# Kernel tuning notes

Measured on AMD Instinct MI355X. Metric: run time of the kernel, lower is better.

Reference implementation:

```python
import jax, jax.numpy as jnp
import numpy as np

EPS = 1e-5
LEAK = 0.1
NPOINT = 4096
NSAMPLE = 32


def setup_inputs() -> dict:
    key = jax.random.key(0)
    ks = jax.random.split(key, 6)
    B, N, Cin = 2, 16384, 64
    ch = [Cin + 3, 64, 64, 128]
    xyz = jax.random.normal(ks[0], (B, 3, N), jnp.float32)
    points = jax.random.normal(ks[1], (B, Cin, N), jnp.float32)
    W0 = jax.random.normal(ks[2], (ch[1], ch[0]), jnp.float32) * 0.05
    W1 = jax.random.normal(ks[3], (ch[2], ch[1]), jnp.float32) * 0.05
    W2 = jax.random.normal(ks[4], (ch[3], ch[2]), jnp.float32) * 0.05
    return dict(
        xyz=xyz, points=points, W0=W0, W1=W1, W2=W2,
        g0=jnp.ones((ch[1],), jnp.float32), b0=jnp.zeros((ch[1],), jnp.float32),
        g1=jnp.ones((ch[2],), jnp.float32), b1=jnp.zeros((ch[2],), jnp.float32),
        g2=jnp.ones((ch[3],), jnp.float32), b2=jnp.zeros((ch[3],), jnp.float32),
    )


def _mlp_bn_act(x, W, g, b):
    # 1x1 conv (no bias) + BatchNorm2d (training: batch stats, biased var) + LeakyReLU(0.1)
    x = jnp.einsum('oc,bcsk->bosk', W, x)
    m = jnp.mean(x, axis=(0, 2, 3), keepdims=True)
    v = jnp.mean(jnp.square(x - m), axis=(0, 2, 3), keepdims=True)
    x = (x - m) * jax.lax.rsqrt(v + EPS) * g[None, :, None, None] + b[None, :, None, None]
    return jnp.where(x >= 0, x, LEAK * x)


def reference(xyz, points, W0, W1, W2, g0, b0, g1, b1, g2, b2):
    B, _, N = xyz.shape
    xyz_t = jnp.transpose(xyz, (0, 2, 1))            # [B,N,3]
    new_xyz = xyz[:, :, :NPOINT]                     # [B,3,S]  (use_fps=False path)
    new_xyz_t = jnp.transpose(new_xyz, (0, 2, 1))    # [B,S,3]

    # squared distances [B,S,N]
    d = (jnp.sum(new_xyz_t ** 2, -1)[:, :, None]
         + jnp.sum(xyz_t ** 2, -1)[:, None, :]
         - 2.0 * jnp.einsum('bsc,bnc->bsn', new_xyz_t, xyz_t))
    _, knn_idx = jax.lax.top_k(-d, NSAMPLE)          # [B,S,K] nearest neighbors

    gather = jax.vmap(lambda arr, idx: arr[idx])     # ([N,C],[S,K]) -> [S,K,C]
    neighbor_xyz = gather(xyz_t, knn_idx)            # [B,S,K,3]
    direction = neighbor_xyz - new_xyz_t[:, :, None, :]
    grouped = gather(jnp.transpose(points, (0, 2, 1)), knn_idx)  # [B,S,K,Cin]

    x = jnp.transpose(jnp.concatenate([direction, grouped], -1), (0, 3, 1, 2))  # [B,Cin+3,S,K]
    x = _mlp_bn_act(x, W0, g0, b0)
    x = _mlp_bn_act(x, W1, g1, b1)
    x = _mlp_bn_act(x, W2, g2, b2)
    new_points = jnp.max(x, axis=-1)                 # [B,128,S] max-pool over nsample
    return new_xyz, new_points
```

## Files before the change

### kernel.cpp

```cpp
#include <hip/hip_runtime.h>
#include <hip/hip_bf16.h>
#include <stdint.h>

#define N_ALL   16384
#define NPOINT  4096
#define KNN_K   32
#define BATCH   2
#define P_TOT   (BATCH*NPOINT*KNN_K)
#define P_TOTF  262144.0f
#define EPSV    1e-5f

typedef __attribute__((ext_vector_type(8))) short bf16x8;
typedef __attribute__((ext_vector_type(4))) float f32x4;

__device__ unsigned short g_knn[P_TOT];
__device__ __attribute__((aligned(16))) float g_pxyzn[BATCH*N_ALL*4];
__device__ __attribute__((aligned(16))) short g_ptb[BATCH*N_ALL*64];
__device__ __attribute__((aligned(16))) short g_x0b[(size_t)P_TOT*64];
__device__ __attribute__((aligned(16))) short g_x1b[(size_t)P_TOT*64];
__device__ __attribute__((aligned(16))) short g_x2b[(size_t)P_TOT*128];
__device__ __attribute__((aligned(16))) float g_mx[(size_t)BATCH*NPOINT*128];
__device__ __attribute__((aligned(16))) float g_mn[(size_t)BATCH*NPOINT*128];
__device__ __attribute__((aligned(16))) short g_Wb0[4*3*64*8];
__device__ __attribute__((aligned(16))) short g_Wb1[4*2*64*8];
__device__ __attribute__((aligned(16))) short g_Wb2[8*2*64*8];
__device__ float g_p0s[4][128];
__device__ float g_p1s[4][128];
__device__ float g_part2[256];

__device__ __forceinline__ float b2f(short s) {
  union { unsigned u; float f; } v; v.u = ((unsigned)(unsigned short)s) << 16; return v.f;
}
__device__ __forceinline__ short f2b(float f) {
  union { float f; unsigned u; } v; v.f = f;
  unsigned u = v.u;
  u += 0x7FFFu + ((u >> 16) & 1u);
  return (short)(u >> 16);
}
__device__ __forceinline__ unsigned pkbf(float a, float b) {
  union { __hip_bfloat162 h; unsigned u; } v;
  v.h = __float22bfloat162_rn(make_float2(a, b));
  return v.u;
}
__device__ __forceinline__ unsigned long long bperm64(unsigned long long v, int byteaddr) {
  int lo = __builtin_amdgcn_ds_bpermute(byteaddr, (int)(unsigned)(v & 0xFFFFFFFFULL));
  int hi = __builtin_amdgcn_ds_bpermute(byteaddr, (int)(unsigned)(v >> 32));
  return (((unsigned long long)(unsigned)hi) << 32) | (unsigned)lo;
}
__device__ __forceinline__ unsigned long long u64min(unsigned long long a, unsigned long long b) {
  return a < b ? a : b;
}
__device__ __forceinline__ unsigned long long selstage(unsigned long long v,
                                                       unsigned long long pv, bool mx) {
  bool lt = v < pv;
  return (lt != mx) ? v : pv;
}

__device__ __forceinline__ void knn_merge32(unsigned long long& vL,
                                            unsigned long long& worst,
                                            unsigned& worst_hi, float& wd,
                                            unsigned long long vB, int hl,
                                            int aX1, int aX2, int aX4, int aX8,
                                            int aX16, int aRev, int aW) {
  vB = selstage(vB, bperm64(vB, aX1),  ((hl & 1) != 0) != ((hl & 2) != 0));
  vB = selstage(vB, bperm64(vB, aX2),  ((hl & 2) != 0) != ((hl & 4) != 0));
  vB = selstage(vB, bperm64(vB, aX1),  ((hl & 1) != 0) != ((hl & 4) != 0));
  vB = selstage(vB, bperm64(vB, aX4),  ((hl & 4) != 0) != ((hl & 8) != 0));
  vB = selstage(vB, bperm64(vB, aX2),  ((hl & 2) != 0) != ((hl & 8) != 0));
  vB = selstage(vB, bperm64(vB, aX1),  ((hl & 1) != 0) != ((hl & 8) != 0));
  vB = selstage(vB, bperm64(vB, aX8),  ((hl & 8) != 0) != ((hl & 16) != 0));
  vB = selstage(vB, bperm64(vB, aX4),  ((hl & 4) != 0) != ((hl & 16) != 0));
  vB = selstage(vB, bperm64(vB, aX2),  ((hl & 2) != 0) != ((hl & 16) != 0));
  vB = selstage(vB, bperm64(vB, aX1),  ((hl & 1) != 0) != ((hl & 16) != 0));
  vB = selstage(vB, bperm64(vB, aX16), (hl & 16) != 0);
  vB = selstage(vB, bperm64(vB, aX8),  (hl & 8) != 0);
  vB = selstage(vB, bperm64(vB, aX4),  (hl & 4) != 0);
  vB = selstage(vB, bperm64(vB, aX2),  (hl & 2) != 0);
  vB = selstage(vB, bperm64(vB, aX1),  (hl & 1) != 0);
  vL = u64min(vL, bperm64(vB, aRev));
  vL = selstage(vL, bperm64(vL, aX16), (hl & 16) != 0);
  vL = selstage(vL, bperm64(vL, aX8),  (hl & 8) != 0);
  vL = selstage(vL, bperm64(vL, aX4),  (hl & 4) != 0);
  vL = selstage(vL, bperm64(vL, aX2),  (hl & 2) != 0);
  vL = selstage(vL, bperm64(vL, aX1),  (hl & 1) != 0);
  worst = bperm64(vL, aW);
  worst_hi = (unsigned)(worst >> 32);
  unsigned wh = worst_hi;
  unsigned ub = (wh & 0x80000000u) ? (wh ^ 0x80000000u) : ~wh;
  wd = (wh == 0xFFFFFFFFu) ? __builtin_inff() : __uint_as_float(ub);
}

__global__ __launch_bounds__(256) void k_setup(const float* __restrict__ xyz,
                                               const float* __restrict__ points,
                                               const float* __restrict__ W0,
                                               const float* __restrict__ W1,
                                               const float* __restrict__ W2,
                                               float* __restrict__ out) {
#pragma clang fp contract(off)
  __shared__ float tile[64][65];
  int blk = blockIdx.x;
  int t = threadIdx.x;
  if (blk < 512) {
    int b  = blk >> 8;
    int n0 = (blk & 255) << 6;
#pragma unroll
    for (int r = 0; r < 16; r++) {
      int lin = r * 256 + t;
      int c = lin >> 6, nn = lin & 63;
      tile[c][nn] = points[((size_t)(b * 64 + c)) * N_ALL + n0 + nn];
    }
    __syncthreads();
#pragma unroll
    for (int r = 0; r < 16; r++) {
      int lin = r * 256 + t;
      int nn = lin >> 6, c = lin & 63;
      g_ptb[((size_t)(b * N_ALL + n0 + nn)) * 64 + c] = f2b(tile[c][nn]);
    }
  } else if (blk < 640) {
    int i = (blk - 512) * 256 + t;
    if (i < 24576) {
      int s = i & 4095;
      int c = (i >> 12) % 3;
      int b = i / 12288;
      out[i] = xyz[(b * 3 + c) * N_ALL + s];
    }
    int b = i >> 14, n = i & 16383;
    const float* xb = xyz + b * 3 * N_ALL;
    float x = xb[n], y = xb[N_ALL + n], z = xb[2 * N_ALL + n];
    float4 p; p.x = x; p.y = y; p.z = z; p.w = x * x + y * y + z * z;
    ((float4*)g_pxyzn)[i] = p;
  } else {
    for (int i = t; i < 4 * 3 * 64 * 8; i += 256) {
      int j = i & 7, lane = (i >> 3) & 63, rest = i >> 9;
      int kt = rest % 3, mt = rest / 3;
      int m = 16 * mt + (lane & 15);
      int k = 32 * kt + (lane >> 4) * 8 + j;
      float v = 0.f;
      if (k < 64) v = W0[m * 67 + 3 + k];
      else if (k < 67) v = W0[m * 67 + (k - 64)];
      g_Wb0[i] = f2b(v);
    }
    for (int i = t; i < 4 * 2 * 64 * 8; i += 256) {
      int j = i & 7, lane = (i >> 3) & 63;
      int kt = (i >> 9) & 1, mt = i >> 10;
      int m = 16 * mt + (lane & 15);
      int k = 32 * kt + (lane >> 4) * 8 + j;
      g_Wb1[i] = f2b(W1[m * 64 + k]);
    }
    for (int i = t; i < 8 * 2 * 64 * 8; i += 256) {
      int j = i & 7, lane = (i >> 3) & 63;
      int kt = (i >> 9) & 1, mt = i >> 10;
      int m = 16 * mt + (lane & 15);
      int k = 32 * kt + (lane >> 4) * 8 + j;
      g_Wb2[i] = f2b(W2[m * 64 + k]);
    }
    float* z0 = &g_p0s[0][0];
    float* z1 = &g_p1s[0][0];
    for (int i = t; i < 512; i += 256) { z0[i] = 0.f; z1[i] = 0.f; }
    g_part2[t] = 0.f;
  }
}

__global__ __launch_bounds__(256, 8) void k_knn() {
#pragma clang fp contract(off)
  __shared__ unsigned long long buf[4][2][64];
  int wv = threadIdx.x >> 6;
  int lane = threadIdx.x & 63;
  int half = lane >> 5;
  int hl = lane & 31;
  int lanebase = lane & 32;
  unsigned long long* bufh = buf[wv][half];

  int qpair = wv >> 1;
  int range = wv & 1;
  int q = blockIdx.x * 4 + qpair * 2 + half;
  int b = q >> 12, s = q & 4095;
  const float4* pb = (const float4*)g_pxyzn + (b << 14);
  float4 qp = pb[s];
  float qx = qp.x, qy = qp.y, qz = qp.z, qn = qp.w;

  int aX1  = (lanebase | (hl ^ 1))  << 2;
  int aX2  = (lanebase | (hl ^ 2))  << 2;
  int aX4  = (lanebase | (hl ^ 4))  << 2;
  int aX8  = (lanebase | (hl ^ 8))  << 2;
  int aX16 = (lanebase | (hl ^ 16)) << 2;
  int aRev = (lanebase | (31 - hl)) << 2;
  int aW   = (lanebase | 31)        << 2;

  unsigned long long vL = ~0ULL;
  unsigned long long worst = ~0ULL;
  unsigned worst_hi = 0xFFFFFFFFu;
  float wd = __builtin_inff();
  int F = 0;

  int base = range << 13;
  for (int n0 = base; n0 < base + 8192; n0 += 128) {
    float4 p0 = pb[n0 + hl];
    float4 p1 = pb[n0 + 32 + hl];
    float4 p2 = pb[n0 + 64 + hl];
    float4 p3 = pb[n0 + 96 + hl];
    float d[4];
    {
      float dt0 = (qx * p0.x + qy * p0.y) + qz * p0.z;
      float dt1 = (qx * p1.x + qy * p1.y) + qz * p1.z;
      float dt2 = (qx * p2.x + qy * p2.y) + qz * p2.z;
      float dt3 = (qx * p3.x + qy * p3.y) + qz * p3.z;
      d[0] = __builtin_fmaf(-2.0f, dt0, qn + p0.w);
      d[1] = __builtin_fmaf(-2.0f, dt1, qn + p1.w);
      d[2] = __builtin_fmaf(-2.0f, dt2, qn + p2.w);
      d[3] = __builtin_fmaf(-2.0f, dt3, qn + p3.w);
    }
    float md = fminf(fminf(d[0], d[1]), fminf(d[2], d[3]));
    if (__ballot(md <= wd)) {
#pragma unroll
      for (int t = 0; t < 4; t++) {
        bool sv = d[t] <= wd;
        unsigned long long bl = __ballot(sv);
        unsigned mb = half ? (unsigned)(bl >> 32) : (unsigned)bl;
        if (sv) {
          unsigned u = __float_as_uint(d[t]);
          u ^= ((unsigned)(((int)u) >> 31)) | 0x80000000u;
          unsigned long long c = (((unsigned long long)u) << 32)
                               | (unsigned)(n0 + 32 * t + hl);
          bufh[F + __popc(mb & ((1u << hl) - 1u))] = c;
        }
        F += __popc(mb);
        if (__ballot(F >= 32)) {
          int take = F >= 32 ? 32 : F;
          unsigned long long vB = (hl < take) ? bufh[hl] : ~0ULL;
          knn_merge32(vL, worst, worst_hi, wd, vB, hl,
                      aX1, aX2, aX4, aX8, aX16, aRev, aW);
          int R = F - take;
          if (hl < R) bufh[hl] = bufh[32 + hl];
          F = R;
        }
      }
    }
  }
  if (__ballot(F > 0)) {
    unsigned long long vB = (hl < F) ? bufh[hl] : ~0ULL;
    knn_merge32(vL, worst, worst_hi, wd, vB, hl, aX1, aX2, aX4, aX8, aX16, aRev, aW);
  }

  bufh[hl] = vL;
  __syncthreads();
  unsigned long long vB = buf[wv ^ 1][half][hl];
  vL = u64min(vL, bperm64(vB, aRev));
  vL = selstage(vL, bperm64(vL, aX16), (hl & 16) != 0);
  vL = selstage(vL, bperm64(vL, aX8),  (hl & 8) != 0);
  vL = selstage(vL, bperm64(vL, aX4),  (hl & 4) != 0);
  vL = selstage(vL, bperm64(vL, aX2),  (hl & 2) != 0);
  vL = selstage(vL, bperm64(vL, aX1),  (hl & 1) != 0);
  if (range == 0)
    g_knn[((size_t)q << 5) | hl] = (unsigned short)(vL & 0xFFFF);
}

__global__ __launch_bounds__(256) void k_l0(const float* __restrict__ xyz) {
  __shared__ __attribute__((aligned(16))) short feats[256][104];
  int t = threadIdx.x;
  int p0 = blockIdx.x * 256;
  {
    int p = p0 + t;
    int idx = g_knn[p];
    int s = (p >> 5) & 4095;
    int b = p >> 17;
    const short* src = g_ptb + ((size_t)((b << 14) + idx) << 6);
#pragma unroll
    for (int i = 0; i < 8; i++)
      ((int4*)&feats[t][0])[i] = ((const int4*)src)[i];
    const float* xb = xyz + b * 3 * N_ALL;
    int4 z; z.x = 0; z.y = 0; z.z = 0; z.w = 0;
    *(int4*)&feats[t][64] = z;
    *(int4*)&feats[t][72] = z;
    *(int4*)&feats[t][80] = z;
    *(int4*)&feats[t][88] = z;
    short4 d3;
    d3.x = f2b(xb[idx] - xb[s]);
    d3.y = f2b(xb[N_ALL + idx] - xb[N_ALL + s]);
    d3.z = f2b(xb[2 * N_ALL + idx] - xb[2 * N_ALL + s]);
    d3.w = 0;
    *(short4*)&feats[t][64] = d3;
  }
  __syncthreads();
  int lane = t & 63, wv = t >> 6;
  int l15 = lane & 15, quad = lane >> 4;
  bf16x8 A[4][3];
#pragma unroll
  for (int mt = 0; mt < 4; mt++)
#pragma unroll
    for (int kt = 0; kt < 3; kt++)
      A[mt][kt] = *(const bf16x8*)(g_Wb0 + (((mt * 3 + kt) * 64 + lane) << 3));
  f32x4 C[4][4];
#pragma unroll
  for (int mt = 0; mt < 4; mt++)
#pragma unroll
    for (int nt = 0; nt < 4; nt++) C[mt][nt] = 0.f;
#pragma unroll
  for (int kt = 0; kt < 3; kt++)
#pragma unroll
    for (int nt = 0; nt < 4; nt++) {
      bf16x8 B = *(const bf16x8*)(&feats[wv * 64 + nt * 16 + l15][kt * 32 + quad * 8]);
#pragma unroll
      for (int mt = 0; mt < 4; mt++)
        C[mt][nt] = __builtin_amdgcn_mfma_f32_16x16x32_bf16(A[mt][kt], B, C[mt][nt], 0, 0, 0);
    }
  float sA[16], qA[16];
#pragma unroll
  for (int i = 0; i < 16; i++) { sA[i] = 0.f; qA[i] = 0.f; }
#pragma unroll
  for (int mt = 0; mt < 4; mt++)
#pragma unroll
    for (int nt = 0; nt < 4; nt++) {
      int p = p0 + wv * 64 + nt * 16 + l15;
      int c0 = mt * 16 + quad * 4;
      uint2 o;
      o.x = pkbf(C[mt][nt][0], C[mt][nt][1]);
      o.y = pkbf(C[mt][nt][2], C[mt][nt][3]);
      *(uint2*)(g_x0b + ((size_t)p << 6) + c0) = o;
      float v0 = __uint_as_float(o.x << 16);
      float v1 = __uint_as_float(o.x & 0xFFFF0000u);
      float v2 = __uint_as_float(o.y << 16);
      float v3 = __uint_as_float(o.y & 0xFFFF0000u);
      int ib = mt * 4;
      sA[ib+0] += v0; qA[ib+0] = fmaf(v0, v0, qA[ib+0]);
      sA[ib+1] += v1; qA[ib+1] = fmaf(v1, v1, qA[ib+1]);
      sA[ib+2] += v2; qA[ib+2] = fmaf(v2, v2, qA[ib+2]);
      sA[ib+3] += v3; qA[ib+3] = fmaf(v3, v3, qA[ib+3]);
    }
  __syncthreads();
  float* red = (float*)&feats[0][0];
  int rb = t * 36;
#pragma unroll
  for (int w = 0; w < 4; w++) {
    float4 vs; vs.x = sA[w*4+0]; vs.y = sA[w*4+1]; vs.z = sA[w*4+2]; vs.w = sA[w*4+3];
    float4 vq; vq.x = qA[w*4+0]; vq.y = qA[w*4+1]; vq.z = qA[w*4+2]; vq.w = qA[w*4+3];
    *(float4*)&red[rb + w*4] = vs;
    *(float4*)&red[rb + 16 + w*4] = vq;
  }
  __syncthreads();
  if (t < 64) {
    int qd = (t >> 2) & 3;
    int i = ((t >> 4) << 2) | (t & 3);
    float S = 0.f, Q = 0.f;
#pragma unroll
    for (int w = 0; w < 4; w++)
#pragma unroll
      for (int l = 0; l < 16; l++) {
        int row = (w * 64 + qd * 16 + l) * 36;
        S += red[row + i];
        Q += red[row + 16 + i];
      }
    float* sh = &g_p0s[blockIdx.x & 3][0];
    atomicAdd(sh + t, S);
    atomicAdd(sh + 64 + t, Q);
  }
}

__global__ __launch_bounds__(256) void k_l1(const float* __restrict__ g0,
                                            const float* __restrict__ b0) {
  __shared__ float scA[64], shA[64];
  __shared__ __attribute__((aligned(16))) float red[256 * 36];
  int t = threadIdx.x;
  if (t < 64) {
    float ps = g_p0s[0][t] + g_p0s[1][t] + g_p0s[2][t] + g_p0s[3][t];
    float pq = g_p0s[0][64+t] + g_p0s[1][64+t] + g_p0s[2][64+t] + g_p0s[3][64+t];
    float m = ps / P_TOTF;
    float v = pq / P_TOTF - m * m;
    float sc = g0[t] / sqrtf(v + EPSV);
    scA[t] = sc; shA[t] = b0[t] - m * sc;
  }
  __syncthreads();
  int lane = t & 63, wv = t >> 6;
  int l15 = lane & 15, quad = lane >> 4;
  int p0 = blockIdx.x * 256 + wv * 64;
  float scv[2][8], shv[2][8];
#pragma unroll
  for (int kt = 0; kt < 2; kt++)
#pragma unroll
    for (int j = 0; j < 8; j++) {
      int c = kt * 32 + quad * 8 + j;
      scv[kt][j] = scA[c]; shv[kt][j] = shA[c];
    }
  bf16x8 A[4][2];
#pragma unroll
  for (int mt = 0; mt < 4; mt++)
#pragma unroll
    for (int kt = 0; kt < 2; kt++)
      A[mt][kt] = *(const bf16x8*)(g_Wb1 + (((mt * 2 + kt) * 64 + lane) << 3));
  f32x4 C[4][4];
#pragma unroll
  for (int mt = 0; mt < 4; mt++)
#pragma unroll
    for (int nt = 0; nt < 4; nt++) C[mt][nt] = 0.f;
#pragma unroll
  for (int kt = 0; kt < 2; kt++)
#pragma unroll
    for (int nt = 0; nt < 4; nt++) {
      const short* src = g_x0b + (((size_t)(p0 + nt * 16 + l15)) << 6) + kt * 32 + quad * 8;
      uint4 raw = *(const uint4*)src;
      bf16x8 B;
      unsigned* Bu = (unsigned*)&B;
      unsigned ru[4] = {raw.x, raw.y, raw.z, raw.w};
#pragma unroll
      for (int jj = 0; jj < 4; jj++) {
        float lo = __uint_as_float(ru[jj] << 16);
        float hi = __uint_as_float(ru[jj] & 0xFFFF0000u);
        float a0 = lo * scv[kt][2*jj]   + shv[kt][2*jj];
        float a1 = hi * scv[kt][2*jj+1] + shv[kt][2*jj+1];
        a0 = fmaxf(a0, 0.1f * a0);
        a1 = fmaxf(a1, 0.1f * a1);
        Bu[jj] = pkbf(a0, a1);
      }
#pragma unroll
      for (int mt = 0; mt < 4; mt++)
        C[mt][nt] = __builtin_amdgcn_mfma_f32_16x16x32_bf16(A[mt][kt], B, C[mt][nt], 0, 0, 0);
    }
  float sA[16], qA[16];
#pragma unroll
  for (int i = 0; i < 16; i++) { sA[i] = 0.f; qA[i] = 0.f; }
#pragma unroll
  for (int mt = 0; mt < 4; mt++)
#pragma unroll
    for (int nt = 0; nt < 4; nt++) {
      int p = p0 + nt * 16 + l15;
      int c0 = mt * 16 + quad * 4;
      uint2 o;
      o.x = pkbf(C[mt][nt][0], C[mt][nt][1]);
      o.y = pkbf(C[mt][nt][2], C[mt][nt][3]);
      *(uint2*)(g_x1b + ((size_t)p << 6) + c0) = o;
      float v0 = __uint_as_float(o.x << 16);
      float v1 = __uint_as_float(o.x & 0xFFFF0000u);
      float v2 = __uint_as_float(o.y << 16);
      float v3 = __uint_as_float(o.y & 0xFFFF0000u);
      int ib = mt * 4;
      sA[ib+0] += v0; qA[ib+0] = fmaf(v0, v0, qA[ib+0]);
      sA[ib+1] += v1; qA[ib+1] = fmaf(v1, v1, qA[ib+1]);
      sA[ib+2] += v2; qA[ib+2] = fmaf(v2, v2, qA[ib+2]);
      sA[ib+3] += v3; qA[ib+3] = fmaf(v3, v3, qA[ib+3]);
    }
  int rb = t * 36;
#pragma unroll
  for (int w = 0; w < 4; w++) {
    float4 vs; vs.x = sA[w*4+0]; vs.y = sA[w*4+1]; vs.z = sA[w*4+2]; vs.w = sA[w*4+3];
    float4 vq; vq.x = qA[w*4+0]; vq.y = qA[w*4+1]; vq.z = qA[w*4+2]; vq.w = qA[w*4+3];
    *(float4*)&red[rb + w*4] = vs;
    *(float4*)&red[rb + 16 + w*4] = vq;
  }
  __syncthreads();
  if (t < 64) {
    int qd = (t >> 2) & 3;
    int i = ((t >> 4) << 2) | (t & 3);
    float S = 0.f, Q = 0.f;
#pragma unroll
    for (int w = 0; w < 4; w++)
#pragma unroll
      for (int l = 0; l < 16; l++) {
        int row = (w * 64 + qd * 16 + l) * 36;
        S += red[row + i];
        Q += red[row + 16 + i];
      }
    float* sh = &g_p1s[blockIdx.x & 3][0];
    atomicAdd(sh + t, S);
    atomicAdd(sh + 64 + t, Q);
  }
}

__global__ __launch_bounds__(256) void k_l2(const float* __restrict__ g1,
                                            const float* __restrict__ b1) {
  __shared__ float scA[64], shA[64];
  int t = threadIdx.x;
  if (t < 64) {
    float ps = g_p1s[0][t] + g_p1s[1][t] + g_p1s[2][t] + g_p1s[3][t];
    float pq = g_p1s[0][64+t] + g_p1s[1][64+t] + g_p1s[2][64+t] + g_p1s[3][64+t];
    float m = ps / P_TOTF;
    float v = pq / P_TOTF - m * m;
    float sc = g1[t] / sqrtf(v + EPSV);
    scA[t] = sc; shA[t] = b1[t] - m * sc;
  }
  __syncthreads();
  int lane = t & 63, wv = t >> 6;
  int l15 = lane & 15, quad = lane >> 4;
  int chh = wv & 1;
  int p0 = blockIdx.x * 128 + (wv >> 1) * 64;
  float scv[2][8], shv[2][8];
#pragma unroll
  for (int kt = 0; kt < 2; kt++)
#pragma unroll
    for (int j = 0; j < 8; j++) {
      int c = kt * 32 + quad * 8 + j;
      scv[kt][j] = scA[c]; shv[kt][j] = shA[c];
    }
  bf16x8 A[4][2];
#pragma unroll
  for (int mt = 0; mt < 4; mt++)
#pragma unroll
    for (int kt = 0; kt < 2; kt++)
      A[mt][kt] = *(const bf16x8*)(g_Wb2 + ((((4 * chh + mt) * 2 + kt) * 64 + lane) << 3));
  f32x4 C[4][4];
#pragma unroll
  for (int mt = 0; mt < 4; mt++)
#pragma unroll
    for (int nt = 0; nt < 4; nt++) C[mt][nt] = 0.f;
#pragma unroll
  for (int kt = 0; kt < 2; kt++)
#pragma unroll
    for (int nt = 0; nt < 4; nt++) {
      const short* src = g_x1b + (((size_t)(p0 + nt * 16 + l15)) << 6) + kt * 32 + quad * 8;
      uint4 raw = *(const uint4*)src;
      bf16x8 B;
      unsigned* Bu = (unsigned*)&B;
      unsigned ru[4] = {raw.x, raw.y, raw.z, raw.w};
#pragma unroll
      for (int jj = 0; jj < 4; jj++) {
        float lo = __uint_as_float(ru[jj] << 16);
        float hi = __uint_as_float(ru[jj] & 0xFFFF0000u);
        float a0 = lo * scv[kt][2*jj]   + shv[kt][2*jj];
        float a1 = hi * scv[kt][2*jj+1] + shv[kt][2*jj+1];
        a0 = fmaxf(a0, 0.1f * a0);
        a1 = fmaxf(a1, 0.1f * a1);
        Bu[jj] = pkbf(a0, a1);
      }
#pragma unroll
      for (int mt = 0; mt < 4; mt++)
        C[mt][nt] = __builtin_amdgcn_mfma_f32_16x16x32_bf16(A[mt][kt], B, C[mt][nt], 0, 0, 0);
    }
#pragma unroll
  for (int mt = 0; mt < 4; mt++)
#pragma unroll
    for (int nt = 0; nt < 4; nt++) {
      int p = p0 + nt * 16 + l15;
      int c0 = (4 * chh + mt) * 16 + quad * 4;
      uint2 o;
      o.x = pkbf(C[mt][nt][0], C[mt][nt][1]);
      o.y = pkbf(C[mt][nt][2], C[mt][nt][3]);
      *(uint2*)(g_x2b + ((size_t)p << 7) + c0) = o;
    }
}

__global__ __launch_bounds__(1024) void k_red128mx(const short* __restrict__ x,
                                                   float* __restrict__ part) {
  __shared__ float sm[32][132], sq[32][132];
  int t = threadIdx.x;
  int cl = t & 31, wv = t >> 5;
  int g = blockIdx.x * 32 + wv;
  size_t pbase = (size_t)g << 5;
  float s0 = 0.f, s1 = 0.f, s2 = 0.f, s3 = 0.f;
  float q0 = 0.f, q1 = 0.f, q2 = 0.f, q3 = 0.f;
  float mx0 = -3.4e38f, mn0 = 3.4e38f, mx1 = -3.4e38f, mn1 = 3.4e38f;
  float mx2 = -3.4e38f, mn2 = 3.4e38f, mx3 = -3.4e38f, mn3 = 3.4e38f;
#pragma unroll
  for (int k = 0; k < 32; k++) {
    uint2 d = *(const uint2*)(x + ((pbase + k) << 7) + cl * 4);
    float a0 = __uint_as_float(d.x << 16);
    float a1 = __uint_as_float(d.x & 0xFFFF0000u);
    float a2 = __uint_as_float(d.y << 16);
    float a3 = __uint_as_float(d.y & 0xFFFF0000u);
    s0 += a0; q0 = fmaf(a0, a0, q0);
    s1 += a1; q1 = fmaf(a1, a1, q1);
    s2 += a2; q2 = fmaf(a2, a2, q2);
    s3 += a3; q3 = fmaf(a3, a3, q3);
    mx0 = fmaxf(mx0, a0); mn0 = fminf(mn0, a0);
    mx1 = fmaxf(mx1, a1); mn1 = fminf(mn1, a1);
    mx2 = fmaxf(mx2, a2); mn2 = fminf(mn2, a2);
    mx3 = fmaxf(mx3, a3); mn3 = fminf(mn3, a3);
  }
  float4 vmx; vmx.x = mx0; vmx.y = mx1; vmx.z = mx2; vmx.w = mx3;
  float4 vmn; vmn.x = mn0; vmn.y = mn1; vmn.z = mn2; vmn.w = mn3;
  *(float4*)(g_mx + ((size_t)g << 7) + cl * 4) = vmx;
  *(float4*)(g_mn + ((size_t)g << 7) + cl * 4) = vmn;
  float4 vs; vs.x = s0; vs.y = s1; vs.z = s2; vs.w = s3;
  float4 vq; vq.x = q0; vq.y = q1; vq.z = q2; vq.w = q3;
  *(float4*)&sm[wv][cl * 4] = vs;
  *(float4*)&sq[wv][cl * 4] = vq;
  __syncthreads();
  if (t < 128) {
    float S = 0.f, Q = 0.f;
#pragma unroll
    for (int r = 0; r < 32; r++) { S += sm[r][t]; Q += sq[r][t]; }
    atomicAdd(part + t, S); atomicAdd(part + 128 + t, Q);
  }
}

__global__ __launch_bounds__(256) void k_epi(const float* __restrict__ g2,
                                             const float* __restrict__ b2,
                                             float* __restrict__ out) {
  __shared__ float scA[128], shA[128];
  __shared__ float res[16][132];
  int t = threadIdx.x;
  if (t < 128) {
    float m = g_part2[t] / P_TOTF;
    float v = g_part2[128 + t] / P_TOTF - m * m;
    float sc = g2[t] / sqrtf(v + EPSV);
    scA[t] = sc; shA[t] = b2[t] - m * sc;
  }
  __syncthreads();
  int cp = t & 63, sl = t >> 6;
  int c0 = cp * 2, c1 = c0 + 1;
  float sc0 = scA[c0], sh0 = shA[c0];
  float sc1 = scA[c1], sh1 = shA[c1];
  int sg0 = blockIdx.x * 16;
  for (int it = 0; it < 4; it++) {
    int sgl = sl * 4 + it;
    size_t off = ((size_t)(sg0 + sgl) << 7) + c0;
    float2 vmx = *(const float2*)(g_mx + off);
    float2 vmn = *(const float2*)(g_mn + off);
    float a0 = (sc0 >= 0.f ? vmx.x : vmn.x) * sc0 + sh0; a0 = fmaxf(a0, 0.1f * a0);
    float a1 = (sc1 >= 0.f ? vmx.y : vmn.y) * sc1 + sh1; a1 = fmaxf(a1, 0.1f * a1);
    res[sgl][c0] = a0; res[sgl][c1] = a1;
  }
  __syncthreads();
  int b = sg0 >> 12, s0 = sg0 & 4095;
#pragma unroll
  for (int w = 0; w < 2; w++) {
    int fidx = t * 2 + w;
    int c = fidx >> 2, qi = fidx & 3;
    float4 o;
    o.x = res[qi * 4 + 0][c];
    o.y = res[qi * 4 + 1][c];
    o.z = res[qi * 4 + 2][c];
    o.w = res[qi * 4 + 3][c];
    *(float4*)(out + 24576 + (((size_t)(b * 128 + c)) << 12) + s0 + qi * 4) = o;
  }
}

extern "C" void kernel_launch(void* const* d_in, const int* in_sizes, int n_in,
                              void* d_out, int out_size, void* d_ws, size_t ws_size,
                              hipStream_t stream) {
  (void)in_sizes; (void)n_in; (void)out_size; (void)d_ws; (void)ws_size;
  const float* xyz    = (const float*)d_in[0];
  const float* points = (const float*)d_in[1];
  const float* W0     = (const float*)d_in[2];
  const float* W1     = (const float*)d_in[3];
  const float* W2     = (const float*)d_in[4];
  const float* g0     = (const float*)d_in[5];
  const float* b0     = (const float*)d_in[6];
  const float* g1     = (const float*)d_in[7];
  const float* b1     = (const float*)d_in[8];
  const float* g2     = (const float*)d_in[9];
  const float* b2     = (const float*)d_in[10];
  float* out = (float*)d_out;

  short *x2b; float *part2;
  hipGetSymbolAddress((void**)&x2b,   HIP_SYMBOL(g_x2b));
  hipGetSymbolAddress((void**)&part2, HIP_SYMBOL(g_part2));

  hipLaunchKernelGGL(k_setup,    dim3(641),  dim3(256),  0, stream, xyz, points, W0, W1, W2, out);
  hipLaunchKernelGGL(k_knn,      dim3(2048), dim3(256),  0, stream);
  hipLaunchKernelGGL(k_l0,       dim3(1024), dim3(256),  0, stream, xyz);
  hipLaunchKernelGGL(k_l1,       dim3(1024), dim3(256),  0, stream, g0, b0);
  hipLaunchKernelGGL(k_l2,       dim3(2048), dim3(256),  0, stream, g1, b1);
  hipLaunchKernelGGL(k_red128mx, dim3(256),  dim3(1024), 0, stream, x2b, part2);
  hipLaunchKernelGGL(k_epi,      dim3(512),  dim3(256),  0, stream, g2, b2, out);
}
```

Baseline: 301.9 us.

## Fuse layer-2 stats and max/min pooling into k_l2 epilogue, drop x2 buffer

The layer-2 GEMM kernel now computes per-channel sum and sum of squares, plus per-group max and min, directly from its MFMA accumulators. Groups are reduced through shared memory, which removes the 64MB bf16 x2 intermediate and the separate k_red128mx kernel. BN partial sums are spread over 8 atomic slots to reduce contention. The cost is extra shared memory (about 37KB) and register pressure in k_l2, which may lower its occupancy.

```diff
diff --git a/kernel.cpp b/kernel.cpp
--- a/kernel.cpp
+++ b/kernel.cpp
@@ -18,7 +18,6 @@
 __device__ __attribute__((aligned(16))) short g_ptb[BATCH*N_ALL*64];
 __device__ __attribute__((aligned(16))) short g_x0b[(size_t)P_TOT*64];
 __device__ __attribute__((aligned(16))) short g_x1b[(size_t)P_TOT*64];
-__device__ __attribute__((aligned(16))) short g_x2b[(size_t)P_TOT*128];
 __device__ __attribute__((aligned(16))) float g_mx[(size_t)BATCH*NPOINT*128];
 __device__ __attribute__((aligned(16))) float g_mn[(size_t)BATCH*NPOINT*128];
 __device__ __attribute__((aligned(16))) short g_Wb0[4*3*64*8];
@@ -26,7 +25,7 @@
 __device__ __attribute__((aligned(16))) short g_Wb2[8*2*64*8];
 __device__ float g_p0s[4][128];
 __device__ float g_p1s[4][128];
-__device__ float g_part2[256];
+__device__ float g_p2s[8][256];
 
 __device__ __forceinline__ float b2f(short s) {
   union { unsigned u; float f; } v; v.u = ((unsigned)(unsigned short)s) << 16; return v.f;
@@ -156,8 +155,9 @@
     }
     float* z0 = &g_p0s[0][0];
     float* z1 = &g_p1s[0][0];
+    float* z2 = &g_p2s[0][0];
     for (int i = t; i < 512; i += 256) { z0[i] = 0.f; z1[i] = 0.f; }
-    g_part2[t] = 0.f;
+    for (int i = t; i < 2048; i += 256) z2[i] = 0.f;
   }
 }
 
@@ -468,6 +468,7 @@
 __global__ __launch_bounds__(256) void k_l2(const float* __restrict__ g1,
                                             const float* __restrict__ b1) {
   __shared__ float scA[64], shA[64];
+  __shared__ __attribute__((aligned(16))) float red[9216];
   int t = threadIdx.x;
   if (t < 64) {
     float ps = g_p1s[0][t] + g_p1s[1][t] + g_p1s[2][t] + g_p1s[3][t];
@@ -524,60 +525,99 @@
       for (int mt = 0; mt < 4; mt++)
         C[mt][nt] = __builtin_amdgcn_mfma_f32_16x16x32_bf16(A[mt][kt], B, C[mt][nt], 0, 0, 0);
     }
+  float sA[16], qA[16];
+  float mxP[2][16], mnP[2][16];
+#pragma unroll
+  for (int i = 0; i < 16; i++) {
+    sA[i] = 0.f; qA[i] = 0.f;
+    mxP[0][i] = -3.4e38f; mnP[0][i] = 3.4e38f;
+    mxP[1][i] = -3.4e38f; mnP[1][i] = 3.4e38f;
+  }
 #pragma unroll
   for (int mt = 0; mt < 4; mt++)
 #pragma unroll
     for (int nt = 0; nt < 4; nt++) {
-      int p = p0 + nt * 16 + l15;
+      unsigned ox = pkbf(C[mt][nt][0], C[mt][nt][1]);
+      unsigned oy = pkbf(C[mt][nt][2], C[mt][nt][3]);
+      float v0 = __uint_as_float(ox << 16);
+      float v1 = __uint_as_float(ox & 0xFFFF0000u);
+      float v2 = __uint_as_float(oy << 16);
+      float v3 = __uint_as_float(oy & 0xFFFF0000u);
+      int ib = mt * 4, sp = nt >> 1;
+      sA[ib+0] += v0; qA[ib+0] = fmaf(v0, v0, qA[ib+0]);
+      sA[ib+1] += v1; qA[ib+1] = fmaf(v1, v1, qA[ib+1]);
+      sA[ib+2] += v2; qA[ib+2] = fmaf(v2, v2, qA[ib+2]);
+      sA[ib+3] += v3; qA[ib+3] = fmaf(v3, v3, qA[ib+3]);
+      mxP[sp][ib+0] = fmaxf(mxP[sp][ib+0], v0); mnP[sp][ib+0] = fminf(mnP[sp][ib+0], v0);
+      mxP[sp][ib+1] = fmaxf(mxP[sp][ib+1], v1); mnP[sp][ib+1] = fminf(mnP[sp][ib+1], v1);
+      mxP[sp][ib+2] = fmaxf(mxP[sp][ib+2], v2); mnP[sp][ib+2] = fminf(mnP[sp][ib+2], v2);
+      mxP[sp][ib+3] = fmaxf(mxP[sp][ib+3], v3); mnP[sp][ib+3] = fminf(mnP[sp][ib+3], v3);
+    }
+  short* mxs = (short*)red;
+  short* mns = mxs + 8448;
+  int sgl0 = (wv >> 1) * 2;
+#pragma unroll
+  for (int sp = 0; sp < 2; sp++)
+#pragma unroll
+    for (int mt = 0; mt < 4; mt++) {
       int c0 = (4 * chh + mt) * 16 + quad * 4;
-      uint2 o;
-      o.x = pkbf(C[mt][nt][0], C[mt][nt][1]);
-      o.y = pkbf(C[mt][nt][2], C[mt][nt][3]);
-      *(uint2*)(g_x2b + ((size_t)p << 7) + c0) = o;
-    }
-}
-
-__global__ __launch_bounds__(1024) void k_red128mx(const short* __restrict__ x,
-                                                   float* __restrict__ part) {
-  __shared__ float sm[32][132], sq[32][132];
-  int t = threadIdx.x;
-  int cl = t & 31, wv = t >> 5;
-  int g = blockIdx.x * 32 + wv;
-  size_t pbase = (size_t)g << 5;
-  float s0 = 0.f, s1 = 0.f, s2 = 0.f, s3 = 0.f;
-  float q0 = 0.f, q1 = 0.f, q2 = 0.f, q3 = 0.f;
-  float mx0 = -3.4e38f, mn0 = 3.4e38f, mx1 = -3.4e38f, mn1 = 3.4e38f;
-  float mx2 = -3.4e38f, mn2 = 3.4e38f, mx3 = -3.4e38f, mn3 = 3.4e38f;
-#pragma unroll
-  for (int k = 0; k < 32; k++) {
-    uint2 d = *(const uint2*)(x + ((pbase + k) << 7) + cl * 4);
-    float a0 = __uint_as_float(d.x << 16);
-    float a1 = __uint_as_float(d.x & 0xFFFF0000u);
-    float a2 = __uint_as_float(d.y << 16);
-    float a3 = __uint_as_float(d.y & 0xFFFF0000u);
-    s0 += a0; q0 = fmaf(a0, a0, q0);
-    s1 += a1; q1 = fmaf(a1, a1, q1);
-    s2 += a2; q2 = fmaf(a2, a2, q2);
-    s3 += a3; q3 = fmaf(a3, a3, q3);
-    mx0 = fmaxf(mx0, a0); mn0 = fminf(mn0, a0);
-    mx1 = fmaxf(mx1, a1); mn1 = fminf(mn1, a1);
-    mx2 = fmaxf(mx2, a2); mn2 = fminf(mn2, a2);
-    mx3 = fmaxf(mx3, a3); mn3 = fminf(mn3, a3);
-  }
-  float4 vmx; vmx.x = mx0; vmx.y = mx1; vmx.z = mx2; vmx.w = mx3;
-  float4 vmn; vmn.x = mn0; vmn.y = mn1; vmn.z = mn2; vmn.w = mn3;
-  *(float4*)(g_mx + ((size_t)g << 7) + cl * 4) = vmx;
-  *(float4*)(g_mn + ((size_t)g << 7) + cl * 4) = vmn;
-  float4 vs; vs.x = s0; vs.y = s1; vs.z = s2; vs.w = s3;
-  float4 vq; vq.x = q0; vq.y = q1; vq.z = q2; vq.w = q3;
-  *(float4*)&sm[wv][cl * 4] = vs;
-  *(float4*)&sq[wv][cl * 4] = vq;
+      int base = ((sgl0 + sp) * 16 + l15) * 132 + c0;
+      short4 m4;
+      m4.x = f2b(mxP[sp][mt*4+0]); m4.y = f2b(mxP[sp][mt*4+1]);
+      m4.z = f2b(mxP[sp][mt*4+2]); m4.w = f2b(mxP[sp][mt*4+3]);
+      *(short4*)&mxs[base] = m4;
+      short4 n4;
+      n4.x = f2b(mnP[sp][mt*4+0]); n4.y = f2b(mnP[sp][mt*4+1]);
+      n4.z = f2b(mnP[sp][mt*4+2]); n4.w = f2b(mnP[sp][mt*4+3]);
+      *(short4*)&mns[base] = n4;
+    }
+  __syncthreads();
+  {
+    int sg = t >> 6, c0 = (t & 63) * 2;
+    float m0 = -3.4e38f, m1 = -3.4e38f, n0 = 3.4e38f, n1 = 3.4e38f;
+#pragma unroll
+    for (int l = 0; l < 16; l++) {
+      unsigned ux = *(const unsigned*)&mxs[(sg * 16 + l) * 132 + c0];
+      m0 = fmaxf(m0, __uint_as_float(ux << 16));
+      m1 = fmaxf(m1, __uint_as_float(ux & 0xFFFF0000u));
+      unsigned un = *(const unsigned*)&mns[(sg * 16 + l) * 132 + c0];
+      n0 = fminf(n0, __uint_as_float(un << 16));
+      n1 = fminf(n1, __uint_as_float(un & 0xFFFF0000u));
+    }
+    int sgg = blockIdx.x * 4 + sg;
+    float2 vmx; vmx.x = m0; vmx.y = m1;
+    float2 vmn; vmn.x = n0; vmn.y = n1;
+    *(float2*)(g_mx + ((size_t)sgg << 7) + c0) = vmx;
+    *(float2*)(g_mn + ((size_t)sgg << 7) + c0) = vmn;
+  }
+  __syncthreads();
+  int rb = t * 36;
+#pragma unroll
+  for (int w = 0; w < 4; w++) {
+    float4 vs; vs.x = sA[w*4+0]; vs.y = sA[w*4+1]; vs.z = sA[w*4+2]; vs.w = sA[w*4+3];
+    float4 vq; vq.x = qA[w*4+0]; vq.y = qA[w*4+1]; vq.z = qA[w*4+2]; vq.w = qA[w*4+3];
+    *(float4*)&red[rb + w*4] = vs;
+    *(float4*)&red[rb + 16 + w*4] = vq;
+  }
   __syncthreads();
   if (t < 128) {
+    int c = t;
+    int ch2 = c >> 6, mt = (c >> 4) & 3, qd = (c >> 2) & 3, j = c & 3;
+    int i = mt * 4 + j;
     float S = 0.f, Q = 0.f;
 #pragma unroll
-    for (int r = 0; r < 32; r++) { S += sm[r][t]; Q += sq[r][t]; }
-    atomicAdd(part + t, S); atomicAdd(part + 128 + t, Q);
+    for (int w = 0; w < 2; w++) {
+      int wvv = ch2 + w * 2;
+#pragma unroll
+      for (int l = 0; l < 16; l++) {
+        int row = (wvv * 64 + qd * 16 + l) * 36;
+        S += red[row + i];
+        Q += red[row + 16 + i];
+      }
+    }
+    float* sh = &g_p2s[blockIdx.x & 7][0];
+    atomicAdd(sh + c, S);
+    atomicAdd(sh + 128 + c, Q);
   }
 }
 
@@ -588,8 +628,11 @@
   __shared__ float res[16][132];
   int t = threadIdx.x;
   if (t < 128) {
-    float m = g_part2[t] / P_TOTF;
-    float v = g_part2[128 + t] / P_TOTF - m * m;
+    float ps = 0.f, pq = 0.f;
+#pragma unroll
+    for (int s = 0; s < 8; s++) { ps += g_p2s[s][t]; pq += g_p2s[s][128 + t]; }
+    float m = ps / P_TOTF;
+    float v = pq / P_TOTF - m * m;
     float sc = g2[t] / sqrtf(v + EPSV);
     scA[t] = sc; shA[t] = b2[t] - m * sc;
   }
@@ -640,15 +683,10 @@
   const float* b2     = (const float*)d_in[10];
   float* out = (float*)d_out;
 
-  short *x2b; float *part2;
-  hipGetSymbolAddress((void**)&x2b,   HIP_SYMBOL(g_x2b));
-  hipGetSymbolAddress((void**)&part2, HIP_SYMBOL(g_part2));
-
-  hipLaunchKernelGGL(k_setup,    dim3(641),  dim3(256),  0, stream, xyz, points, W0, W1, W2, out);
-  hipLaunchKernelGGL(k_knn,      dim3(2048), dim3(256),  0, stream);
-  hipLaunchKernelGGL(k_l0,       dim3(1024), dim3(256),  0, stream, xyz);
-  hipLaunchKernelGGL(k_l1,       dim3(1024), dim3(256),  0, stream, g0, b0);
-  hipLaunchKernelGGL(k_l2,       dim3(2048), dim3(256),  0, stream, g1, b1);
-  hipLaunchKernelGGL(k_red128mx, dim3(256),  dim3(1024), 0, stream, x2b, part2);
-  hipLaunchKernelGGL(k_epi,      dim3(512),  dim3(256),  0, stream, g2, b2, out);
-}
+  hipLaunchKernelGGL(k_setup, dim3(641),  dim3(256), 0, stream, xyz, points, W0, W1, W2, out);
+  hipLaunchKernelGGL(k_knn,   dim3(2048), dim3(256), 0, stream);
+  hipLaunchKernelGGL(k_l0,    dim3(1024), dim3(256), 0, stream, xyz);
+  hipLaunchKernelGGL(k_l1,    dim3(1024), dim3(256), 0, stream, g0, b0);
+  hipLaunchKernelGGL(k_l2,    dim3(2048), dim3(256), 0, stream, g1, b1);
+  hipLaunchKernelGGL(k_epi,   dim3(512),  dim3(256), 0, stream, g2, b2, out);
+}
```

Measured after the change: 289.9 us. 4.0% less time.
